# Optimization experiments

Measured on AMD Instinct MI355X. Metric: run time of the kernel, lower is better.

## Reference

```python
import jax, jax.numpy as jnp
import numpy as np

B, P, G, C = 64, 5000, 300, 20   # images, preds/img, gt/img, num classes
INPUT_SIZE = 512.0
IOU_THRESH = 0.5


def setup_inputs() -> dict:
    key = jax.random.key(0)
    k1, k2, k3, k4, k5, k6, k7 = jax.random.split(key, 7)
    # predictions: [x1,y1,x2,y2,score,cls], boxes normalized to [0,1]
    pxy = jax.random.uniform(k1, (B, P, 2), minval=0.0, maxval=0.8)
    pwh = jax.random.uniform(k2, (B, P, 2), minval=0.02, maxval=0.2)
    score = jax.random.uniform(k3, (B, P, 1))
    pcls = jax.random.randint(k4, (B, P, 1), 0, C).astype(jnp.float32)
    output = jnp.concatenate([pxy, pxy + pwh, score, pcls], axis=-1)
    # ground truth: [x1,y1,x2,y2,cls]
    txy = jax.random.uniform(k5, (B, G, 2), minval=0.0, maxval=0.8)
    twh = jax.random.uniform(k6, (B, G, 2), minval=0.02, maxval=0.2)
    tcls = jax.random.randint(k7, (B, G, 1), 0, C).astype(jnp.float32)
    labels = jnp.concatenate([txy, txy + twh, tcls], axis=-1)
    return {"output": output, "labels": labels}


def reference(output, labels):
    scale = jnp.array([INPUT_SIZE, INPUT_SIZE, INPUT_SIZE, INPUT_SIZE], dtype=output.dtype)

    def match_image(preds, targets):  # preds [P,6], targets [G,5]
        tcls = targets[:, 4]
        tboxes = targets[:, :4] * scale                     # [G,4]
        tarea = (tboxes[:, 2] - tboxes[:, 0]) * (tboxes[:, 3] - tboxes[:, 1])

        def step(detected, pred):
            pbox = pred[:4] * scale
            lt = jnp.maximum(pbox[:2], tboxes[:, :2])       # [G,2]
            rb = jnp.minimum(pbox[2:], tboxes[:, 2:])
            wh = jnp.clip(rb - lt, 0.0)
            inter = wh[:, 0] * wh[:, 1]
            parea = (pbox[2] - pbox[0]) * (pbox[3] - pbox[1])
            ious = inter / (parea + tarea - inter)          # [G]
            cls_mask = tcls == pred[5]
            masked = jnp.where(cls_mask, ious, -1.0)
            bi = jnp.argmax(masked)                          # greedy argmax over same-class gt
            match = ((pred[4] > 0)
                     & jnp.any(cls_mask)
                     & (masked[bi] > IOU_THRESH)
                     & (~detected[bi]))                      # sequential dedup
            detected = detected.at[bi].set(detected[bi] | match)
            return detected, match

        _, correct = jax.lax.scan(step, jnp.zeros(tboxes.shape[0], dtype=bool), preds)
        return correct                                       # [P] bool

    correct = jax.vmap(match_image)(output, labels).astype(output.dtype)  # [B,P]
    # stats: (correct flag, score, predicted class) per prediction; tcls per image
    stats = jnp.stack([correct, output[:, :, 4], output[:, :, 5]], axis=-1)  # [B,P,3]
    tcls = labels[:, :, 4]                                                    # [B,G]
    return stats, tcls
```

## Files before the change

### kernel.cpp

```cpp
#include <hip/hip_runtime.h>
#include <cstdint>

#define B 64
#define P 5000
#define G 300
#define C 20
#define SCALE_F 512.0f
#define IOU_TH 0.5f
#define NTA 1024
#define NWAVE (NTA / 64)
#define SPT ((P + NTA - 1) / NTA)
#define NCHUNK ((G + 63) / 64)
#define SENT 0x7FFFFFFF

#pragma clang fp contract(off)

__global__ __launch_bounds__(NTA, 4) void match_kernel(
    const float* __restrict__ preds,
    const float* __restrict__ labels,
    float* __restrict__ out_stats,
    float* __restrict__ out_tcls)
{
    const int b = blockIdx.x;
    const int tid = threadIdx.x;
    const int lane = tid & 63;
    const int w = tid >> 6;

    __shared__ float4 sb[G];
    __shared__ float  sa[G];
    __shared__ short  ssi[G];
    __shared__ int    chist[NCHUNK][C];
    __shared__ int    so[C + 1];
    __shared__ int    pcnt[C];
    __shared__ int    firstp[G];
    __shared__ unsigned short psorted[P];

    const float* lab = labels + (size_t)b * G * 5;
    const float* prd = preds + (size_t)b * P * 6;

    if (tid < C) pcnt[tid] = 0;
    if (tid < G) firstp[tid] = SENT;

    float tx1 = 0, ty1 = 0, tx2 = 0, ty2 = 0;
    int tc = -1;
    unsigned long long tmask = 0;
    if (tid < NCHUNK * 64) {
        if (tid < G) {
            tx1 = lab[tid * 5 + 0];
            ty1 = lab[tid * 5 + 1];
            tx2 = lab[tid * 5 + 2];
            ty2 = lab[tid * 5 + 3];
            float cf = lab[tid * 5 + 4];
            tc = (int)cf;
            out_tcls[(size_t)b * G + tid] = cf;
        }
        #pragma unroll
        for (int cc = 0; cc < C; ++cc) {
            unsigned long long m = __ballot(tc == cc);
            if (tc == cc) tmask = m;
            if (lane == cc) chist[w][cc] = __popcll(m);
        }
    }

    int myc[SPT];
    #pragma unroll
    for (int k = 0; k < SPT; ++k) {
        myc[k] = -1;
        int p = k * NTA + tid;
        if (p < P) {
            float2 sc = *reinterpret_cast<const float2*>(prd + (size_t)p * 6 + 4);
            myc[k] = (int)sc.y;
            size_t ip3 = ((size_t)b * P + p) * 3;
            out_stats[ip3 + 0] = 0.0f;
            out_stats[ip3 + 1] = sc.x;
            out_stats[ip3 + 2] = sc.y;
        }
    }
    __syncthreads();

    #pragma unroll
    for (int k = 0; k < SPT; ++k)
        if (myc[k] >= 0) atomicAdd(&pcnt[myc[k]], 1);
    __syncthreads();

    if (tid < 64) {
        int run = 0;
        if (lane < C) {
            #pragma unroll
            for (int u = 0; u < NCHUNK; ++u) {
                int t = chist[u][lane]; chist[u][lane] = run; run += t;
            }
        }
        int v = (lane < C) ? run : 0;
        #pragma unroll
        for (int d = 1; d < 32; d <<= 1) {
            int o = __shfl_up(v, d);
            if (lane >= d) v += o;
        }
        if (lane < C) so[lane + 1] = v;
        if (lane == 0) so[0] = 0;
    }
    if (tid == 64) {
        int a = 0;
        for (int c = 0; c < C; ++c) { int v = pcnt[c]; pcnt[c] = a; a += v; }
    }
    __syncthreads();

    if (tid < G) {
        int rank = chist[w][tc] + __popcll(tmask & ((1ull << lane) - 1));
        int pos = so[tc] + rank;
        float x1 = tx1 * SCALE_F;
        float y1 = ty1 * SCALE_F;
        float x2 = tx2 * SCALE_F;
        float y2 = ty2 * SCALE_F;
        sb[pos] = make_float4(x1, y1, x2, y2);
        sa[pos] = (x2 - x1) * (y2 - y1);
        ssi[pos] = (short)tid;
    }
    #pragma unroll
    for (int k = 0; k < SPT; ++k) {
        int p = k * NTA + tid;
        if (p < P) {
            int pos = atomicAdd(&pcnt[myc[k]], 1);
            psorted[pos] = (unsigned short)p;
        }
    }
    __syncthreads();

    #pragma unroll
    for (int k = 0; k < SPT; ++k) {
        int slot = k * NTA + tid;
        if (slot >= P) continue;
        int p = psorted[slot];
        const float* pr = prd + (size_t)p * 6;
        float2 q0 = *reinterpret_cast<const float2*>(pr);
        float2 q1 = *reinterpret_cast<const float2*>(pr + 2);
        float2 q2 = *reinterpret_cast<const float2*>(pr + 4);
        float px1 = q0.x * SCALE_F;
        float py1 = q0.y * SCALE_F;
        float px2 = q1.x * SCALE_F;
        float py2 = q1.y * SCALE_F;
        float score = q2.x;
        int c = (int)q2.y;
        float parea = (px2 - px1) * (py2 - py1);

        int lo = so[c], hi = so[c + 1];
        float best = -1.0f;
        int bi = -1;
        for (int j = lo; j < hi; ++j) {
            float4 tb = sb[j];
            float lx = fmaxf(px1, tb.x);
            float ly = fmaxf(py1, tb.y);
            float rx = fminf(px2, tb.z);
            float ry = fminf(py2, tb.w);
            float wd = fmaxf(rx - lx, 0.0f);
            float ht = fmaxf(ry - ly, 0.0f);
            float inter = wd * ht;
            float uni = (parea + sa[j]) - inter;
            float iou = inter / uni;
            if (iou > best) { best = iou; bi = ssi[j]; }
        }

        bool eligible = (score > 0.0f) && (hi > lo) && (best > IOU_TH);
        if (eligible) atomicMin(&firstp[bi], p);
    }
    __syncthreads();

    if (tid < G) {
        int m = firstp[tid];
        if (m != SENT)
            out_stats[((size_t)b * P + m) * 3] = 1.0f;
    }
}

extern "C" void kernel_launch(void* const* d_in, const int* in_sizes, int n_in,
                              void* d_out, int out_size, void* d_ws, size_t ws_size,
                              hipStream_t stream) {
    const float* output = (const float*)d_in[0];
    const float* labels = (const float*)d_in[1];

    float* out_stats = (float*)d_out;
    float* out_tcls  = (float*)d_out + (size_t)B * P * 3;

    match_kernel<<<dim3(B), NTA, 0, stream>>>(output, labels,
                                              out_stats, out_tcls);
}
```

Measured before the change: 81.06 us.

## Split predictions across blocks per image and resolve first-match in second kernel

Each image's predictions are now split over 8 blocks of 512 threads instead of one 1024-thread block, so the grid grows from 64 to 512 blocks on a GPU with many CUs. The class-sorting of predictions (histogram, atomics, permutation buffer) is removed. Each block writes its per-gt minimum matching prediction index to workspace, and a small second kernel reduces across splits and sets the correct flags. This adds an extra launch, redundant label setup per split, and divergence from unsorted classes in the inner loop.

Measured after the change: 70.41 us. -13.1%, faster.

```diff
diff --git a/kernel.cpp b/kernel.cpp
--- a/kernel.cpp
+++ b/kernel.cpp
@@ -7,9 +7,10 @@
 #define C 20
 #define SCALE_F 512.0f
 #define IOU_TH 0.5f
-#define NTA 1024
-#define NWAVE (NTA / 64)
-#define SPT ((P + NTA - 1) / NTA)
+#define NSPLIT 8
+#define PCHUNK ((P + NSPLIT - 1) / NSPLIT)
+#define NTA 512
+#define SPT ((PCHUNK + NTA - 1) / NTA)
 #define NCHUNK ((G + 63) / 64)
 #define SENT 0x7FFFFFFF
 
@@ -18,27 +19,27 @@
 __global__ __launch_bounds__(NTA, 4) void match_kernel(
     const float* __restrict__ preds,
     const float* __restrict__ labels,
+    int* __restrict__ blockfp,
     float* __restrict__ out_stats,
     float* __restrict__ out_tcls)
 {
-    const int b = blockIdx.x;
+    const int s = blockIdx.x;
+    const int b = blockIdx.y;
     const int tid = threadIdx.x;
     const int lane = tid & 63;
     const int w = tid >> 6;
 
     __shared__ float4 sb[G];
     __shared__ float  sa[G];
-    __shared__ short  ssi[G];
     __shared__ int    chist[NCHUNK][C];
     __shared__ int    so[C + 1];
-    __shared__ int    pcnt[C];
     __shared__ int    firstp[G];
-    __shared__ unsigned short psorted[P];
 
     const float* lab = labels + (size_t)b * G * 5;
     const float* prd = preds + (size_t)b * P * 6;
+    const int pbase = s * PCHUNK;
+    const int pend = (pbase + PCHUNK < P) ? pbase + PCHUNK : P;
 
-    if (tid < C) pcnt[tid] = 0;
     if (tid < G) firstp[tid] = SENT;
 
     float tx1 = 0, ty1 = 0, tx2 = 0, ty2 = 0;
@@ -52,7 +53,7 @@
             ty2 = lab[tid * 5 + 3];
             float cf = lab[tid * 5 + 4];
             tc = (int)cf;
-            out_tcls[(size_t)b * G + tid] = cf;
+            if (s == 0) out_tcls[(size_t)b * G + tid] = cf;
         }
         #pragma unroll
         for (int cc = 0; cc < C; ++cc) {
@@ -61,26 +62,6 @@
             if (lane == cc) chist[w][cc] = __popcll(m);
         }
     }
-
-    int myc[SPT];
-    #pragma unroll
-    for (int k = 0; k < SPT; ++k) {
-        myc[k] = -1;
-        int p = k * NTA + tid;
-        if (p < P) {
-            float2 sc = *reinterpret_cast<const float2*>(prd + (size_t)p * 6 + 4);
-            myc[k] = (int)sc.y;
-            size_t ip3 = ((size_t)b * P + p) * 3;
-            out_stats[ip3 + 0] = 0.0f;
-            out_stats[ip3 + 1] = sc.x;
-            out_stats[ip3 + 2] = sc.y;
-        }
-    }
-    __syncthreads();
-
-    #pragma unroll
-    for (int k = 0; k < SPT; ++k)
-        if (myc[k] >= 0) atomicAdd(&pcnt[myc[k]], 1);
     __syncthreads();
 
     if (tid < 64) {
@@ -100,10 +81,6 @@
         if (lane < C) so[lane + 1] = v;
         if (lane == 0) so[0] = 0;
     }
-    if (tid == 64) {
-        int a = 0;
-        for (int c = 0; c < C; ++c) { int v = pcnt[c]; pcnt[c] = a; a += v; }
-    }
     __syncthreads();
 
     if (tid < G) {
@@ -115,23 +92,13 @@
         float y2 = ty2 * SCALE_F;
         sb[pos] = make_float4(x1, y1, x2, y2);
         sa[pos] = (x2 - x1) * (y2 - y1);
-        ssi[pos] = (short)tid;
-    }
-    #pragma unroll
-    for (int k = 0; k < SPT; ++k) {
-        int p = k * NTA + tid;
-        if (p < P) {
-            int pos = atomicAdd(&pcnt[myc[k]], 1);
-            psorted[pos] = (unsigned short)p;
-        }
     }
     __syncthreads();
 
     #pragma unroll
     for (int k = 0; k < SPT; ++k) {
-        int slot = k * NTA + tid;
-        if (slot >= P) continue;
-        int p = psorted[slot];
+        int p = pbase + k * NTA + tid;
+        if (p >= pend) continue;
         const float* pr = prd + (size_t)p * 6;
         float2 q0 = *reinterpret_cast<const float2*>(pr);
         float2 q1 = *reinterpret_cast<const float2*>(pr + 2);
@@ -143,6 +110,11 @@
         float score = q2.x;
         int c = (int)q2.y;
         float parea = (px2 - px1) * (py2 - py1);
+
+        size_t ip3 = ((size_t)b * P + p) * 3;
+        out_stats[ip3 + 0] = 0.0f;
+        out_stats[ip3 + 1] = score;
+        out_stats[ip3 + 2] = q2.y;
 
         int lo = so[c], hi = so[c + 1];
         float best = -1.0f;
@@ -158,7 +130,7 @@
             float inter = wd * ht;
             float uni = (parea + sa[j]) - inter;
             float iou = inter / uni;
-            if (iou > best) { best = iou; bi = ssi[j]; }
+            if (iou > best) { best = iou; bi = j; }
         }
 
         bool eligible = (score > 0.0f) && (hi > lo) && (best > IOU_TH);
@@ -166,11 +138,25 @@
     }
     __syncthreads();
 
-    if (tid < G) {
-        int m = firstp[tid];
-        if (m != SENT)
-            out_stats[((size_t)b * P + m) * 3] = 1.0f;
-    }
+    if (tid < G)
+        blockfp[((size_t)b * NSPLIT + s) * G + tid] = firstp[tid];
+}
+
+__global__ __launch_bounds__(512) void resolve_kernel(
+    const int* __restrict__ blockfp,
+    float* __restrict__ out_stats)
+{
+    const int b = blockIdx.x;
+    const int t = threadIdx.x;
+    if (t >= G) return;
+
+    const int* fp = blockfp + (size_t)b * NSPLIT * G + t;
+    int m = fp[0];
+    #pragma unroll
+    for (int s = 1; s < NSPLIT; ++s) m = min(m, fp[s * G]);
+
+    if (m != SENT)
+        out_stats[((size_t)b * P + m) * 3] = 1.0f;
 }
 
 extern "C" void kernel_launch(void* const* d_in, const int* in_sizes, int n_in,
@@ -182,6 +168,10 @@
     float* out_stats = (float*)d_out;
     float* out_tcls  = (float*)d_out + (size_t)B * P * 3;
 
-    match_kernel<<<dim3(B), NTA, 0, stream>>>(output, labels,
-                                              out_stats, out_tcls);
+    int* blockfp = (int*)d_ws;
+
+    dim3 grid(NSPLIT, B);
+    match_kernel<<<grid, NTA, 0, stream>>>(output, labels, blockfp,
+                                           out_stats, out_tcls);
+    resolve_kernel<<<dim3(B), 512, 0, stream>>>(blockfp, out_stats);
 }
```
